# Kernel optimization log

Hardware: AMD Instinct MI355X
Metric: run time of the kernel (lower is better)

The kernel has to match this reference:

```python
import jax, jax.numpy as jnp
import numpy as np

N = 100_000            # particles
E = 3_200_000          # edges (avg degree 32)
DIM = 3
H = 1.0                # kernel_radius
SIGMA = 3.0 / 359.0 / np.pi / H**3   # 3D quintic kernel normalization
RHO_REF = 1.0
P_REF = 100.0          # rho_ref * (10*u_ref)**2 / gamma, gamma=1
P_BG = 0.0             # p_bg_factor * p_ref
ETA0 = 0.01            # base_viscosity
EPS = 1e-8


def _qpows(d, p):
    q = d / H
    return (jnp.maximum(0.0, 1.0 - q) ** p,
            jnp.maximum(0.0, 2.0 - q) ** p,
            jnp.maximum(0.0, 3.0 - q) ** p)


def kernel_w(d):
    q1, q2, q3 = _qpows(d, 5)
    return SIGMA * (q3 - 6.0 * q2 + 15.0 * q1)


def kernel_grad_w(d):
    q1, q2, q3 = _qpows(d, 4)
    return (SIGMA / H) * (-5.0 * q3 + 30.0 * q2 - 75.0 * q1)


def setup_inputs() -> dict:
    key = jax.random.key(0)
    k1, k2, k3, k4 = jax.random.split(key, 4)
    r = jax.random.uniform(k1, (N, DIM), dtype=jnp.float32)   # positions in unit box
    v = jax.random.normal(k2, (N, DIM), dtype=jnp.float32)    # velocity history (last frame)
    i_s = jax.random.randint(k3, (E,), 0, N)                  # receivers
    j_s = jax.random.randint(k4, (E,), 0, N)                  # senders
    return {"r": r, "v": v, "i_s": i_s, "j_s": j_s}


def reference(r, v, i_s, j_s):
    n = r.shape[0]
    # --- per-edge gather + kernel ---
    dr = r[i_s] - r[j_s]                       # displacement_fn, [E,3]
    d = jnp.sqrt(jnp.sum(dr * dr, axis=-1))    # [E]
    w = kernel_w(d)
    # --- density summation (scatter) ---
    mass = jnp.ones((n,), r.dtype)
    rho = mass * jax.ops.segment_sum(w, i_s, num_segments=n)
    # Tait EoS, gamma=1
    p = P_REF * (rho / RHO_REF - 1.0) + P_BG
    eta = jnp.full((n,), ETA0, r.dtype)

    # --- per-edge acceleration (gather particle fields to edges) ---
    rho_i, rho_j = rho[i_s], rho[j_s]
    p_i, p_j = p[i_s], p[j_s]
    eta_i, eta_j = eta[i_s], eta[j_s]
    u_i, u_j = v[i_s], v[j_s]                  # u == v in _transform
    v_i, v_j = u_i, u_j

    eta_ij = 2.0 * eta_i * eta_j / (eta_i + eta_j + EPS)
    p_ij = (rho_j * p_i + rho_i * p_j) / (rho_i + rho_j)
    # ((m_i/rho_i)^2 + (m_j/rho_j)^2)/m_i with m == 1
    wvol = (1.0 / rho_i) ** 2 + (1.0 / rho_j) ** 2
    c = wvol * kernel_grad_w(d) / (d + EPS)    # [E]

    # transport stress A = (outer(rho_i*u_i, v_i-u_i) + outer(rho_j*u_j, v_j-u_j))/2, [E,3,3]
    A = 0.5 * (rho_i[:, None, None] * u_i[:, :, None] * (v_i - u_i)[:, None, :]
               + rho_j[:, None, None] * u_j[:, :, None] * (v_j - u_j)[:, None, :])
    Ar = jnp.einsum('eij,ej->ei', A, dr)

    a_eq_8 = c[:, None] * (-p_ij[:, None] * dr + Ar + eta_ij[:, None] * (u_i - u_j))
    p_bg_i = jnp.zeros_like(p_i)               # _transform passes zeros
    a_eq_13 = (c * p_bg_i)[:, None] * dr

    # --- scatter-reduce to particles ---
    dudt = jax.ops.segment_sum(a_eq_8, i_s, num_segments=n)   # [N,3]
    dvdt = jax.ops.segment_sum(a_eq_13, i_s, num_segments=n)  # [N,3]

    # pack state outputs: [rho, p, dudt(3), dvdt(3)] -> [N,8]
    return jnp.concatenate([rho[:, None], p[:, None], dudt, dvdt], axis=1)
```

## Files before the change

### kernel.cpp

```cpp
#include <hip/hip_runtime.h>
#include <math.h>

#ifndef M_PI
#define M_PI 3.14159265358979323846
#endif

static constexpr float kSigma = (float)(3.0 / 359.0 / M_PI);
static constexpr float kPRef  = 100.0f;
static constexpr float kEps   = 1e-8f;
static constexpr float kEta   = (float)(2.0 * 0.01 * 0.01 / (0.01 + 0.01 + 1e-8));

#define CHUNKA 8192

__device__ __forceinline__ float pow5f(float t) { float t2 = t * t; return t2 * t2 * t; }
__device__ __forceinline__ float pow4f(float t) { float t2 = t * t; return t2 * t2; }

__global__ void k_pack(const float* __restrict__ r, float4* __restrict__ pos4,
                       int* __restrict__ offset, int n, int E) {
    int i = blockIdx.x * blockDim.x + threadIdx.x;
    if (i == 0) offset[n] = E;
    if (i >= n) return;
    pos4[i] = make_float4(r[3 * i], r[3 * i + 1], r[3 * i + 2], 0.f);
}

__global__ void k_hist(const int* __restrict__ i_s, int* __restrict__ ghist,
                       int nbA, int E, int shift) {
    __shared__ int h[256];
    int t = threadIdx.x, blk = blockIdx.x;
    h[t] = 0;
    __syncthreads();
    int base = blk * CHUNKA;
    int end = min(base + CHUNKA, E);
    for (int k = base + t; k < end; k += 256)
        atomicAdd(&h[i_s[k] >> shift], 1);
    __syncthreads();
    ghist[t * nbA + blk] = h[t];
}

__global__ void k_scan_block(const int* __restrict__ in, int* __restrict__ out,
                             int* __restrict__ bsum, int m) {
    __shared__ int s[256];
    int t = threadIdx.x;
    int i = blockIdx.x * 256 + t;
    int x = (i < m) ? in[i] : 0;
    s[t] = x;
    __syncthreads();
    for (int d = 1; d < 256; d <<= 1) {
        int v = (t >= d) ? s[t - d] : 0;
        __syncthreads();
        s[t] += v;
        __syncthreads();
    }
    if (i < m) out[i] = s[t] - x;
    if (t == 255) bsum[blockIdx.x] = s[255];
}

__global__ void k_scan_bsums(const int* __restrict__ bsum, int* __restrict__ bscan, int nb) {
    __shared__ int s[512];
    int t = threadIdx.x;
    int x = (t < nb) ? bsum[t] : 0;
    s[t] = x;
    __syncthreads();
    for (int d = 1; d < 512; d <<= 1) {
        int v = (t >= d) ? s[t - d] : 0;
        __syncthreads();
        s[t] += v;
        __syncthreads();
    }
    if (t < nb) bscan[t] = s[t] - x;
}

__global__ void k_scan_add(int* __restrict__ a, const int* __restrict__ bscan, int m) {
    int i = blockIdx.x * blockDim.x + threadIdx.x;
    if (i < m) a[i] += bscan[i >> 8];
}

__global__ void k_split(const int* __restrict__ i_s, const int* __restrict__ j_s,
                        const int* __restrict__ gscan, int2* __restrict__ pairs,
                        int nbA, int E, int shift) {
    __shared__ int cur[256];
    int t = threadIdx.x, blk = blockIdx.x;
    cur[t] = gscan[t * nbA + blk];
    __syncthreads();
    int base = blk * CHUNKA;
    int end = min(base + CHUNKA, E);
    for (int k = base + t; k < end; k += 256) {
        int i = i_s[k];
        int pos = atomicAdd(&cur[i >> shift], 1);
        pairs[pos] = make_int2(i, j_s[k]);
    }
}

__global__ void k_binsort(const int2* __restrict__ pairs, const int* __restrict__ gscan,
                          int* __restrict__ sortedJ, int* __restrict__ offset,
                          int nbA, int n, int E, int shift) {
    __shared__ int h[512];
    __shared__ int se[2];
    int b = blockIdx.x, t = threadIdx.x;
    h[t] = 0;
    if (t == 0) {
        se[0] = gscan[b * nbA];
        int idx = (b + 1) * nbA;
        se[1] = (idx < 256 * nbA) ? gscan[idx] : E;
    }
    __syncthreads();
    int s = se[0], e = se[1];
    int lo = b << shift;
    for (int k = s + t; k < e; k += 512)
        atomicAdd(&h[pairs[k].x - lo], 1);
    __syncthreads();
    int x = h[t];
    for (int d = 1; d < 512; d <<= 1) {
        int v = (t >= d) ? h[t - d] : 0;
        __syncthreads();
        h[t] += v;
        __syncthreads();
    }
    int excl = h[t] - x;
    int i = lo + t;
    if (i < n) offset[i] = s + excl;
    __syncthreads();
    h[t] = s + excl;
    __syncthreads();
    for (int k = s + t; k < e; k += 512) {
        int2 pr = pairs[k];
        int pos = atomicAdd(&h[pr.x - lo], 1);
        sortedJ[pos] = pr.y;
    }
}

__global__ void k_rho(const float4* __restrict__ pos4, const float* __restrict__ v,
                      const int* __restrict__ sortedJ, const int* __restrict__ offset,
                      float4* __restrict__ pv8, float* __restrict__ out, int n) {
    int p = (int)((blockIdx.x * (size_t)blockDim.x + threadIdx.x) >> 5);
    int lane = threadIdx.x & 31;
    if (p >= n) return;
    float4 ri = pos4[p];
    int s = offset[p], e = offset[p + 1];
    float acc = 0.f;
    for (int k = s + lane; k < e; k += 32) {
        int j = sortedJ[k];
        float4 rj = pos4[j];
        float dx = ri.x - rj.x, dy = ri.y - rj.y, dz = ri.z - rj.z;
        float d = sqrtf(dx * dx + dy * dy + dz * dz);
        float t1 = fmaxf(1.f - d, 0.f);
        float t2 = fmaxf(2.f - d, 0.f);
        float t3 = fmaxf(3.f - d, 0.f);
        acc += kSigma * (pow5f(t3) - 6.f * pow5f(t2) + 15.f * pow5f(t1));
    }
    for (int o = 16; o; o >>= 1) acc += __shfl_down(acc, o, 32);
    if (lane == 0) {
        float rh = acc;
        float pp = kPRef * (rh - 1.0f);
        pv8[2 * p]     = make_float4(ri.x, ri.y, ri.z, rh);
        pv8[2 * p + 1] = make_float4(v[3 * p], v[3 * p + 1], v[3 * p + 2], pp);
        float* o = out + (size_t)p * 8;
        o[0] = rh;
        o[1] = pp;
    }
}

__global__ void k_acc(const float4* __restrict__ pv8, const int* __restrict__ sortedJ,
                      const int* __restrict__ offset, float* __restrict__ out, int n) {
    int p = (int)((blockIdx.x * (size_t)blockDim.x + threadIdx.x) >> 5);
    int lane = threadIdx.x & 31;
    if (p >= n) return;
    float4 ai = pv8[2 * p], bi = pv8[2 * p + 1];
    float rho_i = ai.w, p_i = bi.w;
    float inv_i = 1.0f / rho_i;
    float inv2_i = inv_i * inv_i;
    int s = offset[p], e = offset[p + 1];
    float ax = 0.f, ay = 0.f, az = 0.f;
    for (int k = s + lane; k < e; k += 32) {
        int j = sortedJ[k];
        float4 aj = pv8[2 * j];
        float4 bj = pv8[2 * j + 1];
        float rho_j = aj.w, p_j = bj.w;
        float dx = ai.x - aj.x, dy = ai.y - aj.y, dz = ai.z - aj.z;
        float d = sqrtf(dx * dx + dy * dy + dz * dz);
        float t1 = fmaxf(1.f - d, 0.f);
        float t2 = fmaxf(2.f - d, 0.f);
        float t3 = fmaxf(3.f - d, 0.f);
        float gw = kSigma * (-5.f * pow4f(t3) + 30.f * pow4f(t2) - 75.f * pow4f(t1));
        float inv_j = 1.0f / rho_j;
        float c = (inv2_i + inv_j * inv_j) * gw / (d + kEps);
        float p_ij = (rho_j * p_i + rho_i * p_j) / (rho_i + rho_j);
        ax += c * (kEta * (bi.x - bj.x) - p_ij * dx);
        ay += c * (kEta * (bi.y - bj.y) - p_ij * dy);
        az += c * (kEta * (bi.z - bj.z) - p_ij * dz);
    }
    for (int o = 16; o; o >>= 1) {
        ax += __shfl_down(ax, o, 32);
        ay += __shfl_down(ay, o, 32);
        az += __shfl_down(az, o, 32);
    }
    if (lane == 0) {
        float* o = out + (size_t)p * 8 + 2;
        o[0] = ax; o[1] = ay; o[2] = az;
    }
}

static inline char* wcarve(char*& ws, size_t bytes) {
    char* p = ws;
    ws += (bytes + 255) & ~(size_t)255;
    return p;
}

extern "C" void kernel_launch(void* const* d_in, const int* in_sizes, int n_in,
                              void* d_out, int out_size, void* d_ws, size_t ws_size,
                              hipStream_t stream) {
    const float* r = (const float*)d_in[0];
    const float* v = (const float*)d_in[1];
    const int* i_s = (const int*)d_in[2];
    const int* j_s = (const int*)d_in[3];
    int n = in_sizes[0] / 3;
    int E = in_sizes[2];
    float* out = (float*)d_out;

    int shift = 9;
    while ((((n - 1) >> shift) + 1) > 256) shift++;
    int cb_used = ((n - 1) >> shift) + 1;

    int nbA = (E + CHUNKA - 1) / CHUNKA;
    int m = 256 * nbA;
    int nb2 = (m + 255) / 256;

    char* ws = (char*)d_ws;
    float4* pos4   = (float4*)wcarve(ws, (size_t)n * 16);
    float4* pv8    = (float4*)wcarve(ws, (size_t)n * 32);
    int*    offset = (int*)wcarve(ws, (size_t)(n + 1) * 4);
    int*    ghist  = (int*)wcarve(ws, (size_t)m * 4);
    int*    gscan  = (int*)wcarve(ws, (size_t)m * 4);
    int*    bsum   = (int*)wcarve(ws, (size_t)nb2 * 4);
    int*    bscan  = (int*)wcarve(ws, (size_t)nb2 * 4);
    int2*   pairs  = (int2*)wcarve(ws, (size_t)E * 8);
    int*    sortedJ= (int*)wcarve(ws, (size_t)E * 4);

    hipMemsetAsync(out, 0, (size_t)out_size * sizeof(float), stream);

    const int bs = 256;
    int gn = (n + bs - 1) / bs;
    int gp = (n + 7) / 8;

    k_pack<<<gn, bs, 0, stream>>>(r, pos4, offset, n, E);
    k_hist<<<nbA, 256, 0, stream>>>(i_s, ghist, nbA, E, shift);
    k_scan_block<<<nb2, 256, 0, stream>>>(ghist, gscan, bsum, m);
    k_scan_bsums<<<1, 512, 0, stream>>>(bsum, bscan, nb2);
    k_scan_add<<<nb2, 256, 0, stream>>>(gscan, bscan, m);
    k_split<<<nbA, 256, 0, stream>>>(i_s, j_s, gscan, pairs, nbA, E, shift);
    k_binsort<<<cb_used, 512, 0, stream>>>(pairs, gscan, sortedJ, offset, nbA, n, E, shift);
    k_rho<<<gp, bs, 0, stream>>>(pos4, v, sortedJ, offset, pv8, out, n);
    k_acc<<<gp, bs, 0, stream>>>(pv8, sortedJ, offset, out, n);
}
```

Baseline: 209.0 us.

## Pack sort pairs into single ints, use more coarse bins, drop scan-add and memset

The counting sort now uses up to 512 coarse bins of 256 particles each with smaller input chunks, so the per-bin local sort in k_binsort has more blocks and less work per block. Each pair is packed into one 32-bit int (fine index shifted above the receiver bits), which halves the pair-buffer traffic. The separate k_scan_add pass is folded into its consumers. The output memset is replaced by zero writes in k_rho. This raises the histogram size and the number of scan elements, and the packing depends on the fine-index and index bits fitting into 31 bits.

```diff
diff --git a/kernel.cpp b/kernel.cpp
--- a/kernel.cpp
+++ b/kernel.cpp
@@ -10,7 +10,7 @@
 static constexpr float kEps   = 1e-8f;
 static constexpr float kEta   = (float)(2.0 * 0.01 * 0.01 / (0.01 + 0.01 + 1e-8));
 
-#define CHUNKA 8192
+#define CHUNKA 2048
 
 __device__ __forceinline__ float pow5f(float t) { float t2 = t * t; return t2 * t2 * t; }
 __device__ __forceinline__ float pow4f(float t) { float t2 = t * t; return t2 * t2; }
@@ -24,17 +24,18 @@
 }
 
 __global__ void k_hist(const int* __restrict__ i_s, int* __restrict__ ghist,
-                       int nbA, int E, int shift) {
-    __shared__ int h[256];
+                       int nbA, int nbins, int E, int shift) {
+    __shared__ int h[512];
     int t = threadIdx.x, blk = blockIdx.x;
-    h[t] = 0;
+    for (int b = t; b < nbins; b += 256) h[b] = 0;
     __syncthreads();
     int base = blk * CHUNKA;
     int end = min(base + CHUNKA, E);
     for (int k = base + t; k < end; k += 256)
         atomicAdd(&h[i_s[k] >> shift], 1);
     __syncthreads();
-    ghist[t * nbA + blk] = h[t];
+    for (int b = t; b < nbins; b += 256)
+        ghist[b * nbA + blk] = h[b];
 }
 
 __global__ void k_scan_block(const int* __restrict__ in, int* __restrict__ out,
@@ -57,75 +58,88 @@
 
 __global__ void k_scan_bsums(const int* __restrict__ bsum, int* __restrict__ bscan, int nb) {
     __shared__ int s[512];
+    __shared__ int carry;
     int t = threadIdx.x;
-    int x = (t < nb) ? bsum[t] : 0;
-    s[t] = x;
-    __syncthreads();
-    for (int d = 1; d < 512; d <<= 1) {
-        int v = (t >= d) ? s[t - d] : 0;
-        __syncthreads();
-        s[t] += v;
-        __syncthreads();
-    }
-    if (t < nb) bscan[t] = s[t] - x;
-}
-
-__global__ void k_scan_add(int* __restrict__ a, const int* __restrict__ bscan, int m) {
-    int i = blockIdx.x * blockDim.x + threadIdx.x;
-    if (i < m) a[i] += bscan[i >> 8];
+    if (t == 0) carry = 0;
+    __syncthreads();
+    for (int base = 0; base < nb; base += 512) {
+        int i = base + t;
+        int x = (i < nb) ? bsum[i] : 0;
+        s[t] = x;
+        __syncthreads();
+        for (int d = 1; d < 512; d <<= 1) {
+            int v = (t >= d) ? s[t - d] : 0;
+            __syncthreads();
+            s[t] += v;
+            __syncthreads();
+        }
+        if (i < nb) bscan[i] = s[t] - x + carry;
+        __syncthreads();
+        if (t == 511) carry += s[511];
+        __syncthreads();
+    }
 }
 
 __global__ void k_split(const int* __restrict__ i_s, const int* __restrict__ j_s,
-                        const int* __restrict__ gscan, int2* __restrict__ pairs,
-                        int nbA, int E, int shift) {
-    __shared__ int cur[256];
+                        const int* __restrict__ gscan, const int* __restrict__ bscan,
+                        int* __restrict__ pairs, int nbA, int nbins, int E,
+                        int shift, int jbits) {
+    __shared__ int cur[512];
     int t = threadIdx.x, blk = blockIdx.x;
-    cur[t] = gscan[t * nbA + blk];
-    __syncthreads();
+    for (int b = t; b < nbins; b += 256) {
+        int idx = b * nbA + blk;
+        cur[b] = gscan[idx] + bscan[idx >> 8];
+    }
+    __syncthreads();
+    int fmask = (1 << shift) - 1;
     int base = blk * CHUNKA;
     int end = min(base + CHUNKA, E);
     for (int k = base + t; k < end; k += 256) {
         int i = i_s[k];
         int pos = atomicAdd(&cur[i >> shift], 1);
-        pairs[pos] = make_int2(i, j_s[k]);
-    }
-}
-
-__global__ void k_binsort(const int2* __restrict__ pairs, const int* __restrict__ gscan,
-                          int* __restrict__ sortedJ, int* __restrict__ offset,
-                          int nbA, int n, int E, int shift) {
+        pairs[pos] = ((i & fmask) << jbits) | j_s[k];
+    }
+}
+
+__global__ void k_binsort(const int* __restrict__ pairs, const int* __restrict__ gscan,
+                          const int* __restrict__ bscan, int* __restrict__ sortedJ,
+                          int* __restrict__ offset, int nbA, int n, int E,
+                          int shift, int jbits, int m) {
     __shared__ int h[512];
-    __shared__ int se[2];
+    __shared__ int sse[2];
     int b = blockIdx.x, t = threadIdx.x;
-    h[t] = 0;
+    int fine = 1 << shift;
+    if (t < fine) h[t] = 0;
     if (t == 0) {
-        se[0] = gscan[b * nbA];
-        int idx = (b + 1) * nbA;
-        se[1] = (idx < 256 * nbA) ? gscan[idx] : E;
-    }
-    __syncthreads();
-    int s = se[0], e = se[1];
-    int lo = b << shift;
+        int i0 = b * nbA;
+        sse[0] = gscan[i0] + bscan[i0 >> 8];
+        int i1 = (b + 1) * nbA;
+        sse[1] = (i1 < m) ? (gscan[i1] + bscan[i1 >> 8]) : E;
+    }
+    __syncthreads();
+    int s = sse[0], e = sse[1];
+    int jm = (1 << jbits) - 1;
     for (int k = s + t; k < e; k += 512)
-        atomicAdd(&h[pairs[k].x - lo], 1);
-    __syncthreads();
-    int x = h[t];
-    for (int d = 1; d < 512; d <<= 1) {
-        int v = (t >= d) ? h[t - d] : 0;
-        __syncthreads();
-        h[t] += v;
-        __syncthreads();
-    }
-    int excl = h[t] - x;
-    int i = lo + t;
-    if (i < n) offset[i] = s + excl;
-    __syncthreads();
-    h[t] = s + excl;
+        atomicAdd(&h[pairs[k] >> jbits], 1);
+    __syncthreads();
+    int x = (t < fine) ? h[t] : 0;
+    for (int d = 1; d < fine; d <<= 1) {
+        int v = (t >= d && t < fine) ? h[t - d] : 0;
+        __syncthreads();
+        if (t < fine) h[t] += v;
+        __syncthreads();
+    }
+    if (t < fine) {
+        int i = (b << shift) + t;
+        if (i < n) offset[i] = s + h[t] - x;
+    }
+    __syncthreads();
+    if (t < fine) h[t] = s + h[t] - x;
     __syncthreads();
     for (int k = s + t; k < e; k += 512) {
-        int2 pr = pairs[k];
-        int pos = atomicAdd(&h[pr.x - lo], 1);
-        sortedJ[pos] = pr.y;
+        int pr = pairs[k];
+        int pos = atomicAdd(&h[pr >> jbits], 1);
+        sortedJ[pos] = pr & jm;
     }
 }
 
@@ -157,6 +171,7 @@
         float* o = out + (size_t)p * 8;
         o[0] = rh;
         o[1] = pp;
+        o[5] = 0.f; o[6] = 0.f; o[7] = 0.f;
     }
 }
 
@@ -217,12 +232,14 @@
     int E = in_sizes[2];
     float* out = (float*)d_out;
 
-    int shift = 9;
-    while ((((n - 1) >> shift) + 1) > 256) shift++;
-    int cb_used = ((n - 1) >> shift) + 1;
+    int shift = 8;
+    int nbins = ((n - 1) >> shift) + 1;
+    while (nbins > 512) { shift++; nbins = ((n - 1) >> shift) + 1; }
+    int jbits = 1;
+    while ((1 << jbits) < n) jbits++;
 
     int nbA = (E + CHUNKA - 1) / CHUNKA;
-    int m = 256 * nbA;
+    int m = nbins * nbA;
     int nb2 = (m + 255) / 256;
 
     char* ws = (char*)d_ws;
@@ -233,22 +250,19 @@
     int*    gscan  = (int*)wcarve(ws, (size_t)m * 4);
     int*    bsum   = (int*)wcarve(ws, (size_t)nb2 * 4);
     int*    bscan  = (int*)wcarve(ws, (size_t)nb2 * 4);
-    int2*   pairs  = (int2*)wcarve(ws, (size_t)E * 8);
+    int*    pairs  = (int*)wcarve(ws, (size_t)E * 4);
     int*    sortedJ= (int*)wcarve(ws, (size_t)E * 4);
-
-    hipMemsetAsync(out, 0, (size_t)out_size * sizeof(float), stream);
 
     const int bs = 256;
     int gn = (n + bs - 1) / bs;
     int gp = (n + 7) / 8;
 
     k_pack<<<gn, bs, 0, stream>>>(r, pos4, offset, n, E);
-    k_hist<<<nbA, 256, 0, stream>>>(i_s, ghist, nbA, E, shift);
+    k_hist<<<nbA, 256, 0, stream>>>(i_s, ghist, nbA, nbins, E, shift);
     k_scan_block<<<nb2, 256, 0, stream>>>(ghist, gscan, bsum, m);
     k_scan_bsums<<<1, 512, 0, stream>>>(bsum, bscan, nb2);
-    k_scan_add<<<nb2, 256, 0, stream>>>(gscan, bscan, m);
-    k_split<<<nbA, 256, 0, stream>>>(i_s, j_s, gscan, pairs, nbA, E, shift);
-    k_binsort<<<cb_used, 512, 0, stream>>>(pairs, gscan, sortedJ, offset, nbA, n, E, shift);
+    k_split<<<nbA, 256, 0, stream>>>(i_s, j_s, gscan, bscan, pairs, nbA, nbins, E, shift, jbits);
+    k_binsort<<<nbins, 512, 0, stream>>>(pairs, gscan, bscan, sortedJ, offset, nbA, n, E, shift, jbits, m);
     k_rho<<<gp, bs, 0, stream>>>(pos4, v, sortedJ, offset, pv8, out, n);
     k_acc<<<gp, bs, 0, stream>>>(pv8, sortedJ, offset, out, n);
 }
```

New measurement: 214.6 us. 2.7% more time.
